# Performance work log

Hardware: AMD Instinct MI355X
Metric: run time of the kernel (lower is better)

Reference implementation:

```python
import jax, jax.numpy as jnp
import numpy as np

DN = ('NCDHW', 'OIDHW', 'NCDHW')
HIDDEN = 512
VOCAB = 8192


def conv3d_s122(x, w, b):
    # stride (1,2,2), padding 1 on all three spatial-temporal dims
    y = jax.lax.conv_general_dilated(x, w, window_strides=(1, 2, 2),
                                     padding=[(1, 1), (1, 1), (1, 1)],
                                     dimension_numbers=DN)
    return y + b[None, :, None, None, None]


def setup_inputs() -> dict:
    key = jax.random.key(0)
    ks = jax.random.split(key, 9)
    c1, c2 = HIDDEN // 4, HIDDEN // 2
    inp = {
        'video': jax.random.normal(ks[0], (2, 3, 16, 128, 128), dtype=jnp.float32),
        'w1': jax.random.normal(ks[1], (c1, 3, 3, 3, 3), dtype=jnp.float32) * 0.05,
        'b1': jnp.zeros((c1,), dtype=jnp.float32),
        'w2': jax.random.normal(ks[2], (c2, c1, 3, 3, 3), dtype=jnp.float32) * 0.05,
        'b2': jnp.zeros((c2,), dtype=jnp.float32),
        'w3': jax.random.normal(ks[3], (HIDDEN, c2, 3, 3, 3), dtype=jnp.float32) * 0.05,
        'b3': jnp.zeros((HIDDEN,), dtype=jnp.float32),
        'codebook': jax.random.normal(ks[4], (VOCAB, HIDDEN), dtype=jnp.float32),
        'emb_table': jax.random.normal(ks[5], (VOCAB, HIDDEN), dtype=jnp.float32),
        'resolution_level': 0,
    }
    return inp


def reference(video, w1, b1, w2, b2, w3, b3, codebook, emb_table, resolution_level):
    h = jax.nn.relu(conv3d_s122(video, w1, b1))
    h = jax.nn.relu(conv3d_s122(h, w2, b2))
    f = conv3d_s122(h, w3, b3)                       # [B, C, T, H', W']
    B, C = f.shape[0], f.shape[1]
    feats = f.reshape(B, C, -1).transpose(0, 2, 1)   # [B, N, C]
    # squared L2 distances (argmin identical to cdist's sqrt distances)
    f2 = jnp.sum(feats * feats, axis=-1, keepdims=True)          # [B, N, 1]
    c2 = jnp.sum(codebook * codebook, axis=-1)                   # [V]
    dots = jnp.einsum('bnc,vc->bnv', feats, codebook)            # [B, N, V]
    sqdist = f2 + c2[None, None, :] - 2.0 * dots
    tokens = jnp.argmin(sqdist, axis=-1)                         # [B, N] int
    embeddings = emb_table[tokens]                               # [B, N, C]
    return tokens, embeddings
```

## Files before the change

### kernel.cpp

```cpp
#include <hip/hip_runtime.h>

typedef __bf16 bf16x8 __attribute__((ext_vector_type(8)));
typedef float  f32x4  __attribute__((ext_vector_type(4)));

__device__ __forceinline__ unsigned int splitpack(float x) {
  unsigned int u = __float_as_uint(x);
  unsigned int hi = (u + 0x7fffu + ((u >> 16) & 1u)) >> 16;
  float l = x - __uint_as_float(hi << 16);
  unsigned int ul = __float_as_uint(l);
  unsigned int lo = (ul + 0x7fffu + ((ul >> 16) & 1u)) >> 16;
  return hi | (lo << 16);
}

__device__ __forceinline__ void mfma_bf16(f32x4& d, uint4 a, uint4 b) {
  d = __builtin_amdgcn_mfma_f32_16x16x32_bf16(
        __builtin_bit_cast(bf16x8, a), __builtin_bit_cast(bf16x8, b), d, 0, 0, 0);
}


__global__ void conv1_k(const float* __restrict__ in, const float* __restrict__ wgt,
                        const float* __restrict__ bias, unsigned int* __restrict__ h1p) {
  const int tx = threadIdx.x;
  const int w0 = tx * 4;
  const int h  = blockIdx.x * 16 + threadIdx.y;
  const int co0 = blockIdx.y * 8;
  const int bz = blockIdx.z;
  const int b = bz >> 4, t = bz & 15;

  float acc[8][4];
  #pragma unroll
  for (int i = 0; i < 8; ++i) {
    const float bv = bias[co0 + i];
    #pragma unroll
    for (int j = 0; j < 4; ++j) acc[i][j] = bv;
  }
  const int cs = 2 * w0 - 2;

  for (int ci = 0; ci < 3; ++ci) {
    const float* inc = in + (size_t)((b * 3 + ci) * 16) * (128 * 128);
    const float* wc  = wgt + ((size_t)co0 * 3 + ci) * 27;
    #pragma unroll
    for (int kd = 0; kd < 3; ++kd) {
      const int t2 = t - 1 + kd;
      if (t2 < 0 || t2 >= 16) continue;
      const float* ip = inc + t2 * (128 * 128);
      #pragma unroll
      for (int kh = 0; kh < 3; ++kh) {
        const int hh = 2 * h - 1 + kh;
        float v[10];
        if (hh >= 0) {
          const float* r = ip + hh * 128 + cs;
          if (cs >= 0) { float2 u = *(const float2*)r; v[0] = u.x; v[1] = u.y; }
          else         { v[0] = 0.f; v[1] = 0.f; }
          float2 u1 = *(const float2*)(r + 2); v[2] = u1.x; v[3] = u1.y;
          float2 u2 = *(const float2*)(r + 4); v[4] = u2.x; v[5] = u2.y;
          float2 u3 = *(const float2*)(r + 6); v[6] = u3.x; v[7] = u3.y;
          float2 u4 = *(const float2*)(r + 8); v[8] = u4.x; v[9] = u4.y;
        } else {
          #pragma unroll
          for (int z = 0; z < 10; ++z) v[z] = 0.f;
        }
        #pragma unroll
        for (int i = 0; i < 8; ++i) {
          const float* wp = wc + (size_t)i * (3 * 27) + kd * 9 + kh * 3;
          const float wa = wp[0], wb = wp[1], wcc = wp[2];
          #pragma unroll
          for (int wi = 0; wi < 4; ++wi) {
            acc[i][wi] = fmaf(v[1 + 2*wi], wa,  acc[i][wi]);
            acc[i][wi] = fmaf(v[2 + 2*wi], wb,  acc[i][wi]);
            acc[i][wi] = fmaf(v[3 + 2*wi], wcc, acc[i][wi]);
          }
        }
      }
    }
  }
  const int ph = h & 1, rr = h >> 1, cc0 = tx * 2;
  const size_t base0 = (size_t)b * 8388608 + (size_t)blockIdx.y * 524288
                     + (size_t)t * 32768 + (size_t)(ph * 2) * 8192 + (size_t)rr * 256;
  #pragma unroll
  for (int i = 0; i < 8; ++i) {
    unsigned int p0 = splitpack(fmaxf(acc[i][0], 0.f));
    unsigned int p1 = splitpack(fmaxf(acc[i][1], 0.f));
    unsigned int p2 = splitpack(fmaxf(acc[i][2], 0.f));
    unsigned int p3 = splitpack(fmaxf(acc[i][3], 0.f));
    h1p[base0 + cc0 * 8 + i]              = p0;
    h1p[base0 + 8192 + cc0 * 8 + i]       = p1;
    h1p[base0 + (cc0 + 1) * 8 + i]        = p2;
    h1p[base0 + 8192 + (cc0 + 1) * 8 + i] = p3;
  }
}

__global__ void split_w2_k(const float* __restrict__ w2, unsigned short* __restrict__ whi,
                           unsigned short* __restrict__ wlo) {
  unsigned int o = blockIdx.x * 256u + threadIdx.x;
  unsigned int j   = o & 7u;
  unsigned int col = (o >> 3) & 127u;
  unsigned int kg  = (o >> 10) & 3u;
  unsigned int cbk = (o >> 12) & 1u;
  unsigned int cic = (o >> 13) & 3u;
  unsigned int tap = o >> 15;
  unsigned int co = cbk * 128u + col, ci = cic * 32u + kg * 8u + j;
  float x = w2[((size_t)co * 128u + ci) * 27u + tap];
  unsigned int p = splitpack(x);
  whi[o] = (unsigned short)(p & 0xffffu);
  wlo[o] = (unsigned short)(p >> 16);
}

__global__ void split_w3_k(const float* __restrict__ w3, unsigned short* __restrict__ whi,
                           unsigned short* __restrict__ wlo) {
  unsigned int o = blockIdx.x * 256u + threadIdx.x;
  unsigned int j   = o & 7u;
  unsigned int col = (o >> 3) & 127u;
  unsigned int kg  = (o >> 10) & 3u;
  unsigned int cb  = (o >> 12) & 3u;
  unsigned int cic = (o >> 14) & 7u;
  unsigned int tap = o >> 17;
  unsigned int co = cb * 128u + col, ci = cic * 32u + kg * 8u + j;
  float x = w3[((size_t)co * 256u + ci) * 27u + tap];
  unsigned int p = splitpack(x);
  whi[o] = (unsigned short)(p & 0xffffu);
  wlo[o] = (unsigned short)(p >> 16);
}

__global__ void split_cb_k(const float* __restrict__ cb, unsigned short* __restrict__ cbhi,
                           unsigned short* __restrict__ cblo) {
  unsigned int o = blockIdx.x * 256u + threadIdx.x;
  unsigned int j   = o & 7u;
  unsigned int row = (o >> 3) & 127u;
  unsigned int kq  = (o >> 10) & 3u;
  unsigned int kc  = (o >> 12) & 15u;
  unsigned int vb  = o >> 16;
  unsigned int v = vb * 128u + row, k = kc * 32u + kq * 8u + j;
  float x = cb[(size_t)v * 512u + k];
  unsigned int p = splitpack(x);
  cbhi[o] = (unsigned short)(p & 0xffffu);
  cblo[o] = (unsigned short)(p >> 16);
}

__global__ void c2_k(const float* __restrict__ cb, float* __restrict__ c2) {
  const int wid = threadIdx.x >> 6, lane = threadIdx.x & 63;
  const int v = blockIdx.x * 4 + wid;
  const float* row = cb + (size_t)v * 512 + lane * 8;
  float4 a = *(const float4*)row, b = *(const float4*)(row + 4);
  float s = a.x*a.x + a.y*a.y + a.z*a.z + a.w*a.w
          + b.x*b.x + b.y*b.y + b.z*b.z + b.w*b.w;
  #pragma unroll
  for (int off = 32; off; off >>= 1) s += __shfl_down(s, off);
  if (lane == 0) c2[v] = s;
}

#define NCH2 108
#define BUFO 16384
__global__ __launch_bounds__(512) void conv2_mfma_k(
    const unsigned int* __restrict__ xp,
    const unsigned short* __restrict__ whi, const unsigned short* __restrict__ wlo,
    const float* __restrict__ bias,
    unsigned int* __restrict__ h2p) {
  __shared__ __align__(16) unsigned short lds[32768];

  const int tid  = threadIdx.x;
  const int lane = tid & 63;
  const int wid  = tid >> 6;
  const int wm   = wid >> 2, wn = wid & 3;
  const int bid = blockIdx.x;
  const int xcd = bid & 7;
  const int q   = bid >> 3;
  const int cbk = q & 1;
  const int nb  = (q >> 1) & 7;
  const int bt  = xcd + 8 * (q >> 4);
  const int b = bt >> 4, t = bt & 15;

  const int skg = tid >> 7;
  const int sn  = tid & 127;
  const int s_hout = nb * 4 + (sn >> 5);
  const int s_wout = sn & 31;

  const int lc = lane & 15, kgl = lane >> 4;

  f32x4 acc[4][2];
  #pragma unroll
  for (int mf = 0; mf < 4; ++mf)
    #pragma unroll
    for (int nf = 0; nf < 2; ++nf) acc[mf][nf] = (f32x4)(0.f);

  auto issue = [&](int ic, uint4& xa, uint4& xb, uint4& wh, uint4& wl) {
    const int tap = ic >> 2, cic = ic & 3;
    const int kd = tap / 9, r9 = tap % 9;
    const int kh = r9 / 3, kw = r9 % 3;
    const int tt = t + kd - 1;
    const int pl = ((kh != 1) ? 2 : 0) + ((kw != 1) ? 1 : 0);
    const int r  = s_hout + (kh != 0) - 1;
    const int c  = s_wout + (kw != 0) - 1;
    const bool oob = (tt < 0) || (tt > 15) || (r < 0) || (c < 0);
    const int o = b * 8388608 + (cic * 4 + skg) * 524288 + tt * 32768 + pl * 8192 + (r * 32 + c) * 8;
    const unsigned int* src = xp + (oob ? 0 : o);
    uint4 a = *(const uint4*)src, bb = *(const uint4*)(src + 4);
    if (oob) { a = make_uint4(0u,0u,0u,0u); bb = make_uint4(0u,0u,0u,0u); }
    xa = a; xb = bb;
    const size_t slab = ((size_t)((tap * 4 + cic) * 2 + cbk)) << 12;
    wh = *(const uint4*)(whi + slab + tid * 8);
    wl = *(const uint4*)(wlo + slab + tid * 8);
  };

  auto stage = [&](int bo, const uint4& xa, const uint4& xb, const uint4& wh, const uint4& wl) {
    *(uint4*)&lds[bo + tid * 8] = wh;
    *(uint4*)&lds[bo + 4096 + tid * 8] = wl;
    uint4 H, L;
    H.x = (xa.x & 0xffffu) | (xa.y << 16);  L.x = (xa.x >> 16) | (xa.y & 0xffff0000u);
    H.y = (xa.z & 0xffffu) | (xa.w << 16);  L.y = (xa.z >> 16) | (xa.w & 0xffff0000u);
    H.z = (xb.x & 0xffffu) | (xb.y << 16);  L.z = (xb.x >> 16) | (xb.y & 0xffff0000u);
    H.w = (xb.z & 0xffffu) | (xb.w << 16);  L.w = (xb.z >> 16) | (xb.w & 0xffff0000u);
    *(uint4*)&lds[bo + 8192  + (skg * 128 + sn) * 8] = H;
    *(uint4*)&lds[bo + 12288 + (skg * 128 + sn) * 8] = L;
  };

  auto mma = [&](int bo) {
    uint4 ah[4], al[4], bh[2], bl[2];
    #pragma unroll
    for (int mf = 0; mf < 4; ++mf) {
      const int o = bo + kgl * 1024 + (wm * 64 + mf * 16 + lc) * 8;
      ah[mf] = *(const uint4*)&lds[o];
      al[mf] = *(const uint4*)&lds[o + 4096];
    }
    #pragma unroll
    for (int nf = 0; nf < 2; ++nf) {
      const int o = bo + 8192 + kgl * 1024 + (wn * 32 + nf * 16 + lc) * 8;
      bh[nf] = *(const uint4*)&lds[o];
      bl[nf] = *(const uint4*)&lds[o + 4096];
    }
    #pragma unroll
    for (int mf = 0; mf < 4; ++mf)
      #pragma unroll
      for (int nf = 0; nf < 2; ++nf) mfma_bf16(acc[mf][nf], ah[mf], bh[nf]);
    #pragma unroll
    for (int mf = 0; mf < 4; ++mf)
      #pragma unroll
      for (int nf = 0; nf < 2; ++nf) mfma_bf16(acc[mf][nf], ah[mf], bl[nf]);
    #pragma unroll
    for (int mf = 0; mf < 4; ++mf)
      #pragma unroll
      for (int nf = 0; nf < 2; ++nf) mfma_bf16(acc[mf][nf], al[mf], bh[nf]);
  };

  uint4 xa0, xb0, wh0, wl0, xa1, xb1, wh1, wl1;
  issue(0, xa0, xb0, wh0, wl0);
  issue(1, xa1, xb1, wh1, wl1);

  #pragma unroll 1
  for (int ic = 0; ic < NCH2; ic += 2) {
    stage(0, xa0, xb0, wh0, wl0);
    __syncthreads();
    if (ic + 2 < NCH2) issue(ic + 2, xa0, xb0, wh0, wl0);
    mma(0);
    stage(BUFO, xa1, xb1, wh1, wl1);
    __syncthreads();
    if (ic + 3 < NCH2) issue(ic + 3, xa1, xb1, wh1, wl1);
    mma(BUFO);
  }

  const int lr4 = (lane >> 4) * 4;
  #pragma unroll
  for (int mf = 0; mf < 4; ++mf) {
    const int co0g = cbk * 128 + wm * 64 + mf * 16 + lr4;
    const float4 bv = *(const float4*)(bias + co0g);
    const float* bp = (const float*)&bv;
    const size_t gbase = (size_t)(b * 32 + (co0g >> 3)) * 131072 + (size_t)t * 8192 + (co0g & 7);
    #pragma unroll
    for (int nf = 0; nf < 2; ++nf) {
      const int n_l = wn * 32 + nf * 16 + lc;
      const int h_out = nb * 4 + (n_l >> 5);
      const int w_out = n_l & 31;
      const int pl_o = ((h_out & 1) << 1) | (w_out & 1);
      const size_t sp = gbase + (size_t)pl_o * 2048 + (size_t)((h_out >> 1) * 16 + (w_out >> 1)) * 8;
      #pragma unroll
      for (int r = 0; r < 4; ++r) {
        const float x = fmaxf(acc[mf][nf][r] + bp[r], 0.f);
        h2p[sp + r] = splitpack(x);
      }
    }
  }
}

#define NCH 216
__global__ __launch_bounds__(512) void conv3_mfma_k(
    const unsigned int* __restrict__ xp,
    const unsigned short* __restrict__ whi, const unsigned short* __restrict__ wlo,
    const float* __restrict__ bias,
    unsigned short* __restrict__ fhi, unsigned short* __restrict__ flo) {
  __shared__ __align__(16) unsigned short lds[32768];

  const int tid  = threadIdx.x;
  const int lane = tid & 63;
  const int wid  = tid >> 6;
  const int wm   = wid >> 2, wn = wid & 3;
  const int bid = blockIdx.x;
  const int xcd = bid & 7;
  const int q   = bid >> 3;
  const int cb  = q & 3;
  const int hb  = (q >> 2) & 1;
  const int bt  = xcd + 8 * (q >> 3);
  const int b = bt >> 4, t = bt & 15;

  const int skg = tid >> 7;
  const int sn  = tid & 127;
  const int shn = hb * 8 + (sn >> 4);
  const int swn = sn & 15;

  const int lc = lane & 15, kgl = lane >> 4;

  f32x4 acc[4][2];
  #pragma unroll
  for (int mf = 0; mf < 4; ++mf)
    #pragma unroll
    for (int nf = 0; nf < 2; ++nf) acc[mf][nf] = (f32x4)(0.f);

  auto issue = [&](int ic, uint4& xa, uint4& xb, uint4& wh, uint4& wl) {
    const int tap = ic >> 3, cic = ic & 7;
    const int kd = tap / 9, r9 = tap % 9;
    const int kh = r9 / 3, kw = r9 % 3;
    const int tt = t + kd - 1;
    const int pl = ((kh != 1) ? 2 : 0) + ((kw != 1) ? 1 : 0);
    const int r  = shn + (kh != 0) - 1;
    const int c  = swn + (kw != 0) - 1;
    const bool oob = (tt < 0) || (tt > 15) || (r < 0) || (c < 0);
    const int o = b * 4194304 + (cic * 4 + skg) * 131072 + tt * 8192 + pl * 2048 + (r * 16 + c) * 8;
    const unsigned int* src = xp + (oob ? 0 : o);
    uint4 a = *(const uint4*)src, bb = *(const uint4*)(src + 4);
    if (oob) { a = make_uint4(0u,0u,0u,0u); bb = make_uint4(0u,0u,0u,0u); }
    xa = a; xb = bb;
    const size_t slab = ((size_t)((tap * 8 + cic) * 4 + cb)) << 12;
    wh = *(const uint4*)(whi + slab + tid * 8);
    wl = *(const uint4*)(wlo + slab + tid * 8);
  };

  auto stage = [&](int bo, const uint4& xa, const uint4& xb, const uint4& wh, const uint4& wl) {
    *(uint4*)&lds[bo + tid * 8] = wh;
    *(uint4*)&lds[bo + 4096 + tid * 8] = wl;
    uint4 H, L;
    H.x = (xa.x & 0xffffu) | (xa.y << 16);  L.x = (xa.x >> 16) | (xa.y & 0xffff0000u);
    H.y = (xa.z & 0xffffu) | (xa.w << 16);  L.y = (xa.z >> 16) | (xa.w & 0xffff0000u);
    H.z = (xb.x & 0xffffu) | (xb.y << 16);  L.z = (xb.x >> 16) | (xb.y & 0xffff0000u);
    H.w = (xb.z & 0xffffu) | (xb.w << 16);  L.w = (xb.z >> 16) | (xb.w & 0xffff0000u);
    *(uint4*)&lds[bo + 8192  + (skg * 128 + sn) * 8] = H;
    *(uint4*)&lds[bo + 12288 + (skg * 128 + sn) * 8] = L;
  };

  auto mma = [&](int bo) {
    uint4 ah[4], al[4], bh[2], bl[2];
    #pragma unroll
    for (int mf = 0; mf < 4; ++mf) {
      const int o = bo + kgl * 1024 + (wm * 64 + mf * 16 + lc) * 8;
      ah[mf] = *(const uint4*)&lds[o];
      al[mf] = *(const uint4*)&lds[o + 4096];
    }
    #pragma unroll
    for (int nf = 0; nf < 2; ++nf) {
      const int o = bo + 8192 + kgl * 1024 + (wn * 32 + nf * 16 + lc) * 8;
      bh[nf] = *(const uint4*)&lds[o];
      bl[nf] = *(const uint4*)&lds[o + 4096];
    }
    #pragma unroll
    for (int mf = 0; mf < 4; ++mf)
      #pragma unroll
      for (int nf = 0; nf < 2; ++nf) mfma_bf16(acc[mf][nf], ah[mf], bh[nf]);
    #pragma unroll
    for (int mf = 0; mf < 4; ++mf)
      #pragma unroll
      for (int nf = 0; nf < 2; ++nf) mfma_bf16(acc[mf][nf], ah[mf], bl[nf]);
    #pragma unroll
    for (int mf = 0; mf < 4; ++mf)
      #pragma unroll
      for (int nf = 0; nf < 2; ++nf) mfma_bf16(acc[mf][nf], al[mf], bh[nf]);
  };

  uint4 xa0, xb0, wh0, wl0, xa1, xb1, wh1, wl1;
  issue(0, xa0, xb0, wh0, wl0);
  issue(1, xa1, xb1, wh1, wl1);

  #pragma unroll 1
  for (int ic = 0; ic < NCH; ic += 2) {
    stage(0, xa0, xb0, wh0, wl0);
    __syncthreads();
    if (ic + 2 < NCH) issue(ic + 2, xa0, xb0, wh0, wl0);
    mma(0);
    stage(BUFO, xa1, xb1, wh1, wl1);
    __syncthreads();
    if (ic + 3 < NCH) issue(ic + 3, xa1, xb1, wh1, wl1);
    mma(BUFO);
  }

  const int lr4 = (lane >> 4) * 4;
  const int tokb = b * 32 + t * 2 + hb;
  #pragma unroll
  for (int mf = 0; mf < 4; ++mf) {
    const int co0g = cb * 128 + wm * 64 + mf * 16 + lr4;
    const float4 bv = *(const float4*)(bias + co0g);
    const int kc = co0g >> 5, kq = (co0g >> 3) & 3, j0 = co0g & 7;
    #pragma unroll
    for (int nf = 0; nf < 2; ++nf) {
      const int n_l = wn * 32 + nf * 16 + lc;
      const size_t off = (size_t)(tokb * 16 + kc) * 4096 + kq * 1024 + n_l * 8 + j0;
      unsigned int p0 = splitpack(acc[mf][nf][0] + bv.x);
      unsigned int p1 = splitpack(acc[mf][nf][1] + bv.y);
      unsigned int p2 = splitpack(acc[mf][nf][2] + bv.z);
      unsigned int p3 = splitpack(acc[mf][nf][3] + bv.w);
      ushort4 h4, l4;
      h4.x = (unsigned short)(p0 & 0xffffu); l4.x = (unsigned short)(p0 >> 16);
      h4.y = (unsigned short)(p1 & 0xffffu); l4.y = (unsigned short)(p1 >> 16);
      h4.z = (unsigned short)(p2 & 0xffffu); l4.z = (unsigned short)(p2 >> 16);
      h4.w = (unsigned short)(p3 & 0xffffu); l4.w = (unsigned short)(p3 >> 16);
      *(ushort4*)(fhi + off) = h4;
      *(ushort4*)(flo + off) = l4;
    }
  }
}

__global__ __launch_bounds__(512) void vq_mfma_k(
    const unsigned short* __restrict__ fhi, const unsigned short* __restrict__ flo,
    const unsigned short* __restrict__ cbhi, const unsigned short* __restrict__ cblo,
    const float* __restrict__ c2,
    float* __restrict__ pval, int* __restrict__ pidx) {
  __shared__ __align__(16) unsigned short lds[16384];

  const int tid  = threadIdx.x;
  const int lane = tid & 63;
  const int wid  = tid >> 6;
  const int wm   = wid >> 2, wn = wid & 3;
  const int vb = blockIdx.x;
  const int tb = blockIdx.y;
  const int v0 = vb * 128, tok0 = tb * 128;

  const int lc = lane & 15, kgl = lane >> 4;
  const uint4* pAhi[4]; const uint4* pAlo[4];
  #pragma unroll
  for (int mf = 0; mf < 4; ++mf) {
    const int off = kgl * 1024 + (wm * 64 + mf * 16 + lc) * 8;
    pAhi[mf] = (const uint4*)&lds[off];
    pAlo[mf] = (const uint4*)&lds[4096 + off];
  }
  const uint4* pBhi[2]; const uint4* pBlo[2];
  #pragma unroll
  for (int nf = 0; nf < 2; ++nf) {
    const int off = kgl * 1024 + (wn * 32 + nf * 16 + lc) * 8;
    pBhi[nf] = (const uint4*)&lds[8192 + off];
    pBlo[nf] = (const uint4*)&lds[12288 + off];
  }
  uint4* wAhi = (uint4*)&lds[tid * 8];
  uint4* wAlo = (uint4*)&lds[4096 + tid * 8];
  uint4* wBhi = (uint4*)&lds[8192 + tid * 8];
  uint4* wBlo = (uint4*)&lds[12288 + tid * 8];

  f32x4 acc[4][2];
  #pragma unroll
  for (int mf = 0; mf < 4; ++mf)
    #pragma unroll
    for (int nf = 0; nf < 2; ++nf) acc[mf][nf] = (f32x4)(0.f);

  uint4 cah, cal, fbh, fbl;
  auto issue = [&](int kc) {
    const size_t cboff = (size_t)(vb * 16 + kc) * 4096 + tid * 8;
    const size_t foff  = (size_t)(tb * 16 + kc) * 4096 + tid * 8;
    cah = *(const uint4*)(cbhi + cboff);
    cal = *(const uint4*)(cblo + cboff);
    fbh = *(const uint4*)(fhi + foff);
    fbl = *(const uint4*)(flo + foff);
  };

  issue(0);

  for (int kc = 0; kc < 16; ++kc) {
    __syncthreads();
    *wAhi = cah;
    *wAlo = cal;
    *wBhi = fbh;
    *wBlo = fbl;
    __syncthreads();
    if (kc + 1 < 16) issue(kc + 1);

    uint4 ah[4], al[4], bh[2], bl[2];
    #pragma unroll
    for (int mf = 0; mf < 4; ++mf) { ah[mf] = *pAhi[mf]; al[mf] = *pAlo[mf]; }
    #pragma unroll
    for (int nf = 0; nf < 2; ++nf) { bh[nf] = *pBhi[nf]; bl[nf] = *pBlo[nf]; }

    #pragma unroll
    for (int mf = 0; mf < 4; ++mf)
      #pragma unroll
      for (int nf = 0; nf < 2; ++nf) mfma_bf16(acc[mf][nf], ah[mf], bh[nf]);
    #pragma unroll
    for (int mf = 0; mf < 4; ++mf)
      #pragma unroll
      for (int nf = 0; nf < 2; ++nf) mfma_bf16(acc[mf][nf], ah[mf], bl[nf]);
    #pragma unroll
    for (int mf = 0; mf < 4; ++mf)
      #pragma unroll
      for (int nf = 0; nf < 2; ++nf) mfma_bf16(acc[mf][nf], al[mf], bh[nf]);
  }

  float best[2]; int bidx[2];
  best[0] = best[1] = 3.4e38f; bidx[0] = bidx[1] = 0;
  #pragma unroll
  for (int mf = 0; mf < 4; ++mf) {
    float cc[4];
    *(float4*)cc = *(const float4*)(c2 + v0 + wm * 64 + mf * 16 + kgl * 4);
    #pragma unroll
    for (int nf = 0; nf < 2; ++nf) {
      #pragma unroll
      for (int r = 0; r < 4; ++r) {
        const float d = cc[r] - 2.f * acc[mf][nf][r];
        const int vg = v0 + wm * 64 + mf * 16 + kgl * 4 + r;
        if (d < best[nf] || (d == best[nf] && vg < bidx[nf])) { best[nf] = d; bidx[nf] = vg; }
      }
    }
  }
  #pragma unroll
  for (int off = 16; off <= 32; off <<= 1) {
    #pragma unroll
    for (int nf = 0; nf < 2; ++nf) {
      const float ov = __shfl_xor(best[nf], off);
      const int   oi = __shfl_xor(bidx[nf], off);
      if (ov < best[nf] || (ov == best[nf] && oi < bidx[nf])) { best[nf] = ov; bidx[nf] = oi; }
    }
  }
  if (lane < 16) {
    #pragma unroll
    for (int nf = 0; nf < 2; ++nf) {
      const int tok = tok0 + wn * 32 + nf * 16 + lane;
      const int slot = vb * 2 + wm;
      pval[(size_t)tok * 128 + slot] = best[nf];
      pidx[(size_t)tok * 128 + slot] = bidx[nf];
    }
  }
}

__global__ void vq_reduce_k(const float* __restrict__ pval, const int* __restrict__ pidx,
                            int* __restrict__ tokens, float* __restrict__ out_tok) {
  const int tok = blockIdx.x * blockDim.x + threadIdx.x;
  float best = 3.4e38f; int bi = 0;
  for (int s = 0; s < 128; ++s) {
    const float v = pval[(size_t)tok * 128 + s];
    const int idx = pidx[(size_t)tok * 128 + s];
    if (v < best || (v == best && idx < bi)) { best = v; bi = idx; }
  }
  tokens[tok] = bi;
  out_tok[tok] = (float)bi;
}

__global__ void gather_k(const int* __restrict__ tokens, const float* __restrict__ emb,
                         float* __restrict__ out) {
  const int i = blockIdx.x * blockDim.x + threadIdx.x;
  const int n = i >> 7;
  const int c4 = (i & 127) * 4;
  const int tk = tokens[n];
  float4 v = *(const float4*)(emb + (size_t)tk * 512 + c4);
  *(float4*)(out + (size_t)n * 512 + c4) = v;
}

extern "C" void kernel_launch(void* const* d_in, const int* in_sizes, int n_in,
                              void* d_out, int out_size, void* d_ws, size_t ws_size,
                              hipStream_t stream) {
  const float* video = (const float*)d_in[0];
  const float* w1 = (const float*)d_in[1];
  const float* b1 = (const float*)d_in[2];
  const float* w2 = (const float*)d_in[3];
  const float* b2 = (const float*)d_in[4];
  const float* w3 = (const float*)d_in[5];
  const float* b3 = (const float*)d_in[6];
  const float* cb  = (const float*)d_in[7];
  const float* emb = (const float*)d_in[8];

  float* ws = (float*)d_ws;
  unsigned int* h1p = (unsigned int*)ws;
  unsigned short* fhi = (unsigned short*)(ws);
  unsigned short* flo = (unsigned short*)(ws + 2097152);
  unsigned short* cbhi = (unsigned short*)(ws + 4194304);
  unsigned short* cblo = (unsigned short*)(ws + 6291456);
  float* c2v  = ws + 8388608;
  float* pval = ws + 8396800;
  int*   pidx = (int*)(ws + 9445376);
  int*   tokens = (int*)(ws + 10493952);
  unsigned int* h2p = (unsigned int*)(ws + 16777216);
  unsigned short* w2hi = (unsigned short*)d_out;
  unsigned short* w2lo = w2hi + 884736;
  unsigned short* w3hi = (unsigned short*)d_out;
  unsigned short* w3lo = w3hi + 3538944;
  float* out_tok = (float*)d_out;
  float* out_emb = (float*)d_out + 8192;

  hipLaunchKernelGGL(conv1_k, dim3(4, 16, 32), dim3(16, 16), 0, stream, video, w1, b1, h1p);
  hipLaunchKernelGGL(split_w2_k, dim3(3456), dim3(256), 0, stream, w2, w2hi, w2lo);
  hipLaunchKernelGGL(conv2_mfma_k, dim3(512), dim3(512), 0, stream,
                     h1p, w2hi, w2lo, b2, h2p);
  hipLaunchKernelGGL(split_w3_k, dim3(13824), dim3(256), 0, stream, w3, w3hi, w3lo);
  hipLaunchKernelGGL(split_cb_k, dim3(16384), dim3(256), 0, stream, cb, cbhi, cblo);
  hipLaunchKernelGGL(c2_k, dim3(2048), dim3(256), 0, stream, cb, c2v);
  hipLaunchKernelGGL(conv3_mfma_k, dim3(256), dim3(512), 0, stream,
                     h2p, w3hi, w3lo, b3, fhi, flo);
  hipLaunchKernelGGL(vq_mfma_k, dim3(64, 64), dim3(512), 0, stream,
                     fhi, flo, cbhi, cblo, c2v, pval, pidx);
  hipLaunchKernelGGL(vq_reduce_k, dim3(32), dim3(256), 0, stream, pval, pidx, tokens, out_tok);
  hipLaunchKernelGGL(gather_k, dim3(4096), dim3(256), 0, stream, tokens, emb, out_emb);
}
```

Before: 749.7 us.

## Use direct global-to-LDS loads with split hi/lo activation planes

Activations from conv1 and conv2 are now stored as separate bf16 hi and lo planes instead of interleaved packed words. This lets conv2, conv3 and the VQ GEMM stage tiles straight into LDS with global_load_lds, skipping the register round trip and the repack shuffles. The VQ kernel moves to a double-buffered LDS pipeline, and out-of-bounds taps point at a small zeroed buffer filled by an extra tiny kernel. The risks are ordering of the asynchronous LDS writes against the barriers and the larger LDS footprint in the VQ kernel.

```diff
diff --git a/kernel.cpp b/kernel.cpp
--- a/kernel.cpp
+++ b/kernel.cpp
@@ -17,9 +17,16 @@
         __builtin_bit_cast(bf16x8, a), __builtin_bit_cast(bf16x8, b), d, 0, 0, 0);
 }
 
+__device__ __forceinline__ void glds16(const void* g, void* l) {
+  __builtin_amdgcn_global_load_lds(
+      (const __attribute__((address_space(1))) unsigned int*)g,
+      (__attribute__((address_space(3))) unsigned int*)l, 16, 0, 0);
+}
+
 
 __global__ void conv1_k(const float* __restrict__ in, const float* __restrict__ wgt,
-                        const float* __restrict__ bias, unsigned int* __restrict__ h1p) {
+                        const float* __restrict__ bias,
+                        unsigned short* __restrict__ h1h, unsigned short* __restrict__ h1l) {
   const int tx = threadIdx.x;
   const int w0 = tx * 4;
   const int h  = blockIdx.x * 16 + threadIdx.y;
@@ -78,15 +85,18 @@
   const size_t base0 = (size_t)b * 8388608 + (size_t)blockIdx.y * 524288
                      + (size_t)t * 32768 + (size_t)(ph * 2) * 8192 + (size_t)rr * 256;
   #pragma unroll
-  for (int i = 0; i < 8; ++i) {
-    unsigned int p0 = splitpack(fmaxf(acc[i][0], 0.f));
-    unsigned int p1 = splitpack(fmaxf(acc[i][1], 0.f));
-    unsigned int p2 = splitpack(fmaxf(acc[i][2], 0.f));
-    unsigned int p3 = splitpack(fmaxf(acc[i][3], 0.f));
-    h1p[base0 + cc0 * 8 + i]              = p0;
-    h1p[base0 + 8192 + cc0 * 8 + i]       = p1;
-    h1p[base0 + (cc0 + 1) * 8 + i]        = p2;
-    h1p[base0 + 8192 + (cc0 + 1) * 8 + i] = p3;
+  for (int pos = 0; pos < 4; ++pos) {
+    const size_t idx = base0 + ((pos & 1) ? 8192 : 0) + (size_t)(cc0 + (pos >> 1)) * 8;
+    unsigned int hw[4], lw[4];
+    #pragma unroll
+    for (int ii = 0; ii < 4; ++ii) {
+      unsigned int pa = splitpack(fmaxf(acc[2*ii][pos], 0.f));
+      unsigned int pb = splitpack(fmaxf(acc[2*ii+1][pos], 0.f));
+      hw[ii] = (pa & 0xffffu) | ((pb & 0xffffu) << 16);
+      lw[ii] = (pa >> 16) | (pb & 0xffff0000u);
+    }
+    *(uint4*)(h1h + idx) = make_uint4(hw[0], hw[1], hw[2], hw[3]);
+    *(uint4*)(h1l + idx) = make_uint4(lw[0], lw[1], lw[2], lw[3]);
   }
 }
 
@@ -149,13 +159,16 @@
   if (lane == 0) c2[v] = s;
 }
 
+__global__ void zero16_k(unsigned int* __restrict__ p) { p[threadIdx.x] = 0u; }
+
 #define NCH2 108
 #define BUFO 16384
 __global__ __launch_bounds__(512) void conv2_mfma_k(
-    const unsigned int* __restrict__ xp,
+    const unsigned short* __restrict__ xh, const unsigned short* __restrict__ xl,
     const unsigned short* __restrict__ whi, const unsigned short* __restrict__ wlo,
+    const unsigned short* __restrict__ zp,
     const float* __restrict__ bias,
-    unsigned int* __restrict__ h2p) {
+    unsigned short* __restrict__ h2h, unsigned short* __restrict__ h2l) {
   __shared__ __align__(16) unsigned short lds[32768];
 
   const int tid  = threadIdx.x;
@@ -183,7 +196,7 @@
     #pragma unroll
     for (int nf = 0; nf < 2; ++nf) acc[mf][nf] = (f32x4)(0.f);
 
-  auto issue = [&](int ic, uint4& xa, uint4& xb, uint4& wh, uint4& wl) {
+  auto issue = [&](int ic, int bo) {
     const int tap = ic >> 2, cic = ic & 3;
     const int kd = tap / 9, r9 = tap % 9;
     const int kh = r9 / 3, kw = r9 % 3;
@@ -193,25 +206,13 @@
     const int c  = s_wout + (kw != 0) - 1;
     const bool oob = (tt < 0) || (tt > 15) || (r < 0) || (c < 0);
     const int o = b * 8388608 + (cic * 4 + skg) * 524288 + tt * 32768 + pl * 8192 + (r * 32 + c) * 8;
-    const unsigned int* src = xp + (oob ? 0 : o);
-    uint4 a = *(const uint4*)src, bb = *(const uint4*)(src + 4);
-    if (oob) { a = make_uint4(0u,0u,0u,0u); bb = make_uint4(0u,0u,0u,0u); }
-    xa = a; xb = bb;
     const size_t slab = ((size_t)((tap * 4 + cic) * 2 + cbk)) << 12;
-    wh = *(const uint4*)(whi + slab + tid * 8);
-    wl = *(const uint4*)(wlo + slab + tid * 8);
-  };
-
-  auto stage = [&](int bo, const uint4& xa, const uint4& xb, const uint4& wh, const uint4& wl) {
-    *(uint4*)&lds[bo + tid * 8] = wh;
-    *(uint4*)&lds[bo + 4096 + tid * 8] = wl;
-    uint4 H, L;
-    H.x = (xa.x & 0xffffu) | (xa.y << 16);  L.x = (xa.x >> 16) | (xa.y & 0xffff0000u);
-    H.y = (xa.z & 0xffffu) | (xa.w << 16);  L.y = (xa.z >> 16) | (xa.w & 0xffff0000u);
-    H.z = (xb.x & 0xffffu) | (xb.y << 16);  L.z = (xb.x >> 16) | (xb.y & 0xffff0000u);
-    H.w = (xb.z & 0xffffu) | (xb.w << 16);  L.w = (xb.z >> 16) | (xb.w & 0xffff0000u);
-    *(uint4*)&lds[bo + 8192  + (skg * 128 + sn) * 8] = H;
-    *(uint4*)&lds[bo + 12288 + (skg * 128 + sn) * 8] = L;
+    glds16(whi + slab + tid * 8, &lds[bo + tid * 8]);
+    glds16(wlo + slab + tid * 8, &lds[bo + 4096 + tid * 8]);
+    const unsigned short* sh = oob ? zp : (xh + o);
+    const unsigned short* sl = oob ? zp : (xl + o);
+    glds16(sh, &lds[bo + 8192 + tid * 8]);
+    glds16(sl, &lds[bo + 12288 + tid * 8]);
   };
 
   auto mma = [&](int bo) {
@@ -242,19 +243,14 @@
       for (int nf = 0; nf < 2; ++nf) mfma_bf16(acc[mf][nf], al[mf], bh[nf]);
   };
 
-  uint4 xa0, xb0, wh0, wl0, xa1, xb1, wh1, wl1;
-  issue(0, xa0, xb0, wh0, wl0);
-  issue(1, xa1, xb1, wh1, wl1);
-
+  issue(0, 0);
   #pragma unroll 1
   for (int ic = 0; ic < NCH2; ic += 2) {
-    stage(0, xa0, xb0, wh0, wl0);
     __syncthreads();
-    if (ic + 2 < NCH2) issue(ic + 2, xa0, xb0, wh0, wl0);
+    if (ic + 1 < NCH2) issue(ic + 1, BUFO);
     mma(0);
-    stage(BUFO, xa1, xb1, wh1, wl1);
     __syncthreads();
-    if (ic + 3 < NCH2) issue(ic + 3, xa1, xb1, wh1, wl1);
+    if (ic + 2 < NCH2) issue(ic + 2, 0);
     mma(BUFO);
   }
 
@@ -272,19 +268,24 @@
       const int w_out = n_l & 31;
       const int pl_o = ((h_out & 1) << 1) | (w_out & 1);
       const size_t sp = gbase + (size_t)pl_o * 2048 + (size_t)((h_out >> 1) * 16 + (w_out >> 1)) * 8;
-      #pragma unroll
-      for (int r = 0; r < 4; ++r) {
-        const float x = fmaxf(acc[mf][nf][r] + bp[r], 0.f);
-        h2p[sp + r] = splitpack(x);
-      }
+      unsigned int qv[4];
+      #pragma unroll
+      for (int r = 0; r < 4; ++r) qv[r] = splitpack(fmaxf(acc[mf][nf][r] + bp[r], 0.f));
+      ushort4 h4 = make_ushort4((unsigned short)(qv[0] & 0xffffu), (unsigned short)(qv[1] & 0xffffu),
+                                (unsigned short)(qv[2] & 0xffffu), (unsigned short)(qv[3] & 0xffffu));
+      ushort4 l4 = make_ushort4((unsigned short)(qv[0] >> 16), (unsigned short)(qv[1] >> 16),
+                                (unsigned short)(qv[2] >> 16), (unsigned short)(qv[3] >> 16));
+      *(ushort4*)(h2h + sp) = h4;
+      *(ushort4*)(h2l + sp) = l4;
     }
   }
 }
 
 #define NCH 216
 __global__ __launch_bounds__(512) void conv3_mfma_k(
-    const unsigned int* __restrict__ xp,
+    const unsigned short* __restrict__ xh, const unsigned short* __restrict__ xl,
     const unsigned short* __restrict__ whi, const unsigned short* __restrict__ wlo,
+    const unsigned short* __restrict__ zp,
     const float* __restrict__ bias,
     unsigned short* __restrict__ fhi, unsigned short* __restrict__ flo) {
   __shared__ __align__(16) unsigned short lds[32768];
@@ -314,7 +315,7 @@
     #pragma unroll
     for (int nf = 0; nf < 2; ++nf) acc[mf][nf] = (f32x4)(0.f);
 
-  auto issue = [&](int ic, uint4& xa, uint4& xb, uint4& wh, uint4& wl) {
+  auto issue = [&](int ic, int bo) {
     const int tap = ic >> 3, cic = ic & 7;
     const int kd = tap / 9, r9 = tap % 9;
     const int kh = r9 / 3, kw = r9 % 3;
@@ -324,25 +325,13 @@
     const int c  = swn + (kw != 0) - 1;
     const bool oob = (tt < 0) || (tt > 15) || (r < 0) || (c < 0);
     const int o = b * 4194304 + (cic * 4 + skg) * 131072 + tt * 8192 + pl * 2048 + (r * 16 + c) * 8;
-    const unsigned int* src = xp + (oob ? 0 : o);
-    uint4 a = *(const uint4*)src, bb = *(const uint4*)(src + 4);
-    if (oob) { a = make_uint4(0u,0u,0u,0u); bb = make_uint4(0u,0u,0u,0u); }
-    xa = a; xb = bb;
     const size_t slab = ((size_t)((tap * 8 + cic) * 4 + cb)) << 12;
-    wh = *(const uint4*)(whi + slab + tid * 8);
-    wl = *(const uint4*)(wlo + slab + tid * 8);
-  };
-
-  auto stage = [&](int bo, const uint4& xa, const uint4& xb, const uint4& wh, const uint4& wl) {
-    *(uint4*)&lds[bo + tid * 8] = wh;
-    *(uint4*)&lds[bo + 4096 + tid * 8] = wl;
-    uint4 H, L;
-    H.x = (xa.x & 0xffffu) | (xa.y << 16);  L.x = (xa.x >> 16) | (xa.y & 0xffff0000u);
-    H.y = (xa.z & 0xffffu) | (xa.w << 16);  L.y = (xa.z >> 16) | (xa.w & 0xffff0000u);
-    H.z = (xb.x & 0xffffu) | (xb.y << 16);  L.z = (xb.x >> 16) | (xb.y & 0xffff0000u);
-    H.w = (xb.z & 0xffffu) | (xb.w << 16);  L.w = (xb.z >> 16) | (xb.w & 0xffff0000u);
-    *(uint4*)&lds[bo + 8192  + (skg * 128 + sn) * 8] = H;
-    *(uint4*)&lds[bo + 12288 + (skg * 128 + sn) * 8] = L;
+    glds16(whi + slab + tid * 8, &lds[bo + tid * 8]);
+    glds16(wlo + slab + tid * 8, &lds[bo + 4096 + tid * 8]);
+    const unsigned short* sh = oob ? zp : (xh + o);
+    const unsigned short* sl = oob ? zp : (xl + o);
+    glds16(sh, &lds[bo + 8192 + tid * 8]);
+    glds16(sl, &lds[bo + 12288 + tid * 8]);
   };
 
   auto mma = [&](int bo) {
@@ -373,19 +362,14 @@
       for (int nf = 0; nf < 2; ++nf) mfma_bf16(acc[mf][nf], al[mf], bh[nf]);
   };
 
-  uint4 xa0, xb0, wh0, wl0, xa1, xb1, wh1, wl1;
-  issue(0, xa0, xb0, wh0, wl0);
-  issue(1, xa1, xb1, wh1, wl1);
-
+  issue(0, 0);
   #pragma unroll 1
   for (int ic = 0; ic < NCH; ic += 2) {
-    stage(0, xa0, xb0, wh0, wl0);
     __syncthreads();
-    if (ic + 2 < NCH) issue(ic + 2, xa0, xb0, wh0, wl0);
+    if (ic + 1 < NCH) issue(ic + 1, BUFO);
     mma(0);
-    stage(BUFO, xa1, xb1, wh1, wl1);
     __syncthreads();
-    if (ic + 3 < NCH) issue(ic + 3, xa1, xb1, wh1, wl1);
+    if (ic + 2 < NCH) issue(ic + 2, 0);
     mma(BUFO);
   }
 
@@ -420,7 +404,7 @@
     const unsigned short* __restrict__ cbhi, const unsigned short* __restrict__ cblo,
     const float* __restrict__ c2,
     float* __restrict__ pval, int* __restrict__ pidx) {
-  __shared__ __align__(16) unsigned short lds[16384];
+  __shared__ __align__(16) unsigned short lds[32768];
 
   const int tid  = threadIdx.x;
   const int lane = tid & 63;
@@ -431,24 +415,6 @@
   const int v0 = vb * 128, tok0 = tb * 128;
 
   const int lc = lane & 15, kgl = lane >> 4;
-  const uint4* pAhi[4]; const uint4* pAlo[4];
-  #pragma unroll
-  for (int mf = 0; mf < 4; ++mf) {
-    const int off = kgl * 1024 + (wm * 64 + mf * 16 + lc) * 8;
-    pAhi[mf] = (const uint4*)&lds[off];
-    pAlo[mf] = (const uint4*)&lds[4096 + off];
-  }
-  const uint4* pBhi[2]; const uint4* pBlo[2];
-  #pragma unroll
-  for (int nf = 0; nf < 2; ++nf) {
-    const int off = kgl * 1024 + (wn * 32 + nf * 16 + lc) * 8;
-    pBhi[nf] = (const uint4*)&lds[8192 + off];
-    pBlo[nf] = (const uint4*)&lds[12288 + off];
-  }
-  uint4* wAhi = (uint4*)&lds[tid * 8];
-  uint4* wAlo = (uint4*)&lds[4096 + tid * 8];
-  uint4* wBhi = (uint4*)&lds[8192 + tid * 8];
-  uint4* wBlo = (uint4*)&lds[12288 + tid * 8];
 
   f32x4 acc[4][2];
   #pragma unroll
@@ -456,45 +422,52 @@
     #pragma unroll
     for (int nf = 0; nf < 2; ++nf) acc[mf][nf] = (f32x4)(0.f);
 
-  uint4 cah, cal, fbh, fbl;
-  auto issue = [&](int kc) {
+  auto issue = [&](int kc, int bo) {
     const size_t cboff = (size_t)(vb * 16 + kc) * 4096 + tid * 8;
     const size_t foff  = (size_t)(tb * 16 + kc) * 4096 + tid * 8;
-    cah = *(const uint4*)(cbhi + cboff);
-    cal = *(const uint4*)(cblo + cboff);
-    fbh = *(const uint4*)(fhi + foff);
-    fbl = *(const uint4*)(flo + foff);
+    glds16(cbhi + cboff, &lds[bo + tid * 8]);
+    glds16(cblo + cboff, &lds[bo + 4096 + tid * 8]);
+    glds16(fhi + foff,  &lds[bo + 8192 + tid * 8]);
+    glds16(flo + foff,  &lds[bo + 12288 + tid * 8]);
   };
 
-  issue(0);
-
-  for (int kc = 0; kc < 16; ++kc) {
+  auto mma = [&](int bo) {
+    uint4 ah[4], al[4], bh[2], bl[2];
+    #pragma unroll
+    for (int mf = 0; mf < 4; ++mf) {
+      const int o = bo + kgl * 1024 + (wm * 64 + mf * 16 + lc) * 8;
+      ah[mf] = *(const uint4*)&lds[o];
+      al[mf] = *(const uint4*)&lds[o + 4096];
+    }
+    #pragma unroll
+    for (int nf = 0; nf < 2; ++nf) {
+      const int o = bo + 8192 + kgl * 1024 + (wn * 32 + nf * 16 + lc) * 8;
+      bh[nf] = *(const uint4*)&lds[o];
+      bl[nf] = *(const uint4*)&lds[o + 4096];
+    }
+    #pragma unroll
+    for (int mf = 0; mf < 4; ++mf)
+      #pragma unroll
+      for (int nf = 0; nf < 2; ++nf) mfma_bf16(acc[mf][nf], ah[mf], bh[nf]);
+    #pragma unroll
+    for (int mf = 0; mf < 4; ++mf)
+      #pragma unroll
+      for (int nf = 0; nf < 2; ++nf) mfma_bf16(acc[mf][nf], ah[mf], bl[nf]);
+    #pragma unroll
+    for (int mf = 0; mf < 4; ++mf)
+      #pragma unroll
+      for (int nf = 0; nf < 2; ++nf) mfma_bf16(acc[mf][nf], al[mf], bh[nf]);
+  };
+
+  issue(0, 0);
+  #pragma unroll 1
+  for (int kc = 0; kc < 16; kc += 2) {
     __syncthreads();
-    *wAhi = cah;
-    *wAlo = cal;
-    *wBhi = fbh;
-    *wBlo = fbl;
+    if (kc + 1 < 16) issue(kc + 1, BUFO);
+    mma(0);
     __syncthreads();
-    if (kc + 1 < 16) issue(kc + 1);
-
-    uint4 ah[4], al[4], bh[2], bl[2];
-    #pragma unroll
-    for (int mf = 0; mf < 4; ++mf) { ah[mf] = *pAhi[mf]; al[mf] = *pAlo[mf]; }
-    #pragma unroll
-    for (int nf = 0; nf < 2; ++nf) { bh[nf] = *pBhi[nf]; bl[nf] = *pBlo[nf]; }
-
-    #pragma unroll
-    for (int mf = 0; mf < 4; ++mf)
-      #pragma unroll
-      for (int nf = 0; nf < 2; ++nf) mfma_bf16(acc[mf][nf], ah[mf], bh[nf]);
-    #pragma unroll
-    for (int mf = 0; mf < 4; ++mf)
-      #pragma unroll
-      for (int nf = 0; nf < 2; ++nf) mfma_bf16(acc[mf][nf], ah[mf], bl[nf]);
-    #pragma unroll
-    for (int mf = 0; mf < 4; ++mf)
-      #pragma unroll
-      for (int nf = 0; nf < 2; ++nf) mfma_bf16(acc[mf][nf], al[mf], bh[nf]);
+    if (kc + 2 < 16) issue(kc + 2, 0);
+    mma(BUFO);
   }
 
   float best[2]; int bidx[2];
@@ -570,7 +543,8 @@
   const float* emb = (const float*)d_in[8];
 
   float* ws = (float*)d_ws;
-  unsigned int* h1p = (unsigned int*)ws;
+  unsigned short* h1h = (unsigned short*)ws;
+  unsigned short* h1l = (unsigned short*)(ws + 8388608);
   unsigned short* fhi = (unsigned short*)(ws);
   unsigned short* flo = (unsigned short*)(ws + 2097152);
   unsigned short* cbhi = (unsigned short*)(ws + 4194304);
@@ -579,7 +553,9 @@
   float* pval = ws + 8396800;
   int*   pidx = (int*)(ws + 9445376);
   int*   tokens = (int*)(ws + 10493952);
-  unsigned int* h2p = (unsigned int*)(ws + 16777216);
+  unsigned short* h2h = (unsigned short*)(ws + 16777216);
+  unsigned short* h2l = (unsigned short*)(ws + 20971520);
+  unsigned short* zp  = (unsigned short*)(ws + 25165824);
   unsigned short* w2hi = (unsigned short*)d_out;
   unsigned short* w2lo = w2hi + 884736;
   unsigned short* w3hi = (unsigned short*)d_out;
@@ -587,15 +563,16 @@
   float* out_tok = (float*)d_out;
   float* out_emb = (float*)d_out + 8192;
 
-  hipLaunchKernelGGL(conv1_k, dim3(4, 16, 32), dim3(16, 16), 0, stream, video, w1, b1, h1p);
+  hipLaunchKernelGGL(conv1_k, dim3(4, 16, 32), dim3(16, 16), 0, stream, video, w1, b1, h1h, h1l);
   hipLaunchKernelGGL(split_w2_k, dim3(3456), dim3(256), 0, stream, w2, w2hi, w2lo);
+  hipLaunchKernelGGL(zero16_k, dim3(1), dim3(16), 0, stream, (unsigned int*)zp);
   hipLaunchKernelGGL(conv2_mfma_k, dim3(512), dim3(512), 0, stream,
-                     h1p, w2hi, w2lo, b2, h2p);
+                     h1h, h1l, w2hi, w2lo, zp, b2, h2h, h2l);
   hipLaunchKernelGGL(split_w3_k, dim3(13824), dim3(256), 0, stream, w3, w3hi, w3lo);
   hipLaunchKernelGGL(split_cb_k, dim3(16384), dim3(256), 0, stream, cb, cbhi, cblo);
   hipLaunchKernelGGL(c2_k, dim3(2048), dim3(256), 0, stream, cb, c2v);
   hipLaunchKernelGGL(conv3_mfma_k, dim3(256), dim3(512), 0, stream,
-                     h2p, w3hi, w3lo, b3, fhi, flo);
+                     h2h, h2l, w3hi, w3lo, zp, b3, fhi, flo);
   hipLaunchKernelGGL(vq_mfma_k, dim3(64, 64), dim3(512), 0, stream,
                      fhi, flo, cbhi, cblo, c2v, pval, pidx);
   hipLaunchKernelGGL(vq_reduce_k, dim3(32), dim3(256), 0, stream, pval, pidx, tokens, out_tok);
```

Measured after the change: 760.7 us. No clear change (+1.5%).
